# Optimization experiments

Measured on AMD Instinct MI355X. Metric: run time of the kernel, lower is better.

The kernel has to match this reference:

```python
import jax, jax.numpy as jnp
import numpy as np

B, S, D, H = 2, 2048, 1024, 16
DK = D // H


def setup_inputs() -> dict:
    key = jax.random.key(0)
    ks = jax.random.split(key, 11)
    s = 1.0 / np.sqrt(D)
    inp = {
        "q": jax.random.normal(ks[0], (B, S, D), jnp.float32),
        "k": jax.random.normal(ks[1], (B, S, D), jnp.float32),
        "v": jax.random.normal(ks[2], (B, S, D), jnp.float32),
        "mask": jnp.tril(jnp.ones((S, S), jnp.int32))[None, None],  # causal [1,1,S,S]
        "w_q": jax.random.normal(ks[3], (D, D), jnp.float32) * s,
        "b_q": jax.random.normal(ks[4], (D,), jnp.float32) * 0.01,
        "w_k": jax.random.normal(ks[5], (D, D), jnp.float32) * s,
        "b_k": jax.random.normal(ks[6], (D,), jnp.float32) * 0.01,
        "w_v": jax.random.normal(ks[7], (D, D), jnp.float32) * s,
        "b_v": jax.random.normal(ks[8], (D,), jnp.float32) * 0.01,
        "w_o": jax.random.normal(ks[9], (D, D), jnp.float32) * s,
        "b_o": jax.random.normal(ks[10], (D,), jnp.float32) * 0.01,
    }
    return inp


def reference(q, k, v, mask, w_q, b_q, w_k, b_k, w_v, b_v, w_o, b_o):
    # Linear projections (torch Linear: x @ W.T + b)
    query = q @ w_q.T + b_q  # [B,S,D]
    key_ = k @ w_k.T + b_k
    value = v @ w_v.T + b_v
    # split heads -> [B,H,S,DK]
    def split(x):
        return x.reshape(B, S, H, DK).transpose(0, 2, 1, 3)
    qh, kh, vh = split(query), split(key_), split(value)
    scores = jnp.einsum("bhqd,bhkd->bhqk", qh, kh) / jnp.sqrt(jnp.float32(DK))
    scores = jnp.where(mask == 0, jnp.float32(-1e9), scores)
    attn = jax.nn.softmax(scores, axis=-1)
    out = jnp.einsum("bhqk,bhkd->bhqd", attn, vh)  # [B,H,S,DK]
    out = out.transpose(0, 2, 1, 3).reshape(B, S, D)
    return out @ w_o.T + b_o
```

## Files before the change

kernel.cpp:

```cpp
#include <hip/hip_runtime.h>


typedef __attribute__((ext_vector_type(8))) short bf16x8;
typedef __attribute__((ext_vector_type(4))) float floatx4;
typedef __attribute__((ext_vector_type(4))) unsigned short u16x4;

#define S_LEN 2048
#define D_MODEL 1024
#define N_HEADS 16
#define D_HEAD 64
#define M_ROWS 4096
#define QSCALE 0.18033688011112042f

#define XSTR 1088
#define VSTR 4160

__device__ __forceinline__ unsigned short f32_to_bf16(float f) {
  unsigned int u = __builtin_bit_cast(unsigned int, f);
  u += 0x7FFFu + ((u >> 16) & 1u);
  return (unsigned short)(u >> 16);
}

__device__ __forceinline__ void async_lds16(const unsigned short* g, unsigned short* l) {
  __builtin_amdgcn_global_load_lds(
      (const __attribute__((address_space(1))) unsigned int*)g,
      (__attribute__((address_space(3))) unsigned int*)l, 16, 0, 0);
}

__global__ __launch_bounds__(256) void cvt_w(
    const float* __restrict__ w0, const float* __restrict__ w1,
    const float* __restrict__ w2, const float* __restrict__ w3,
    unsigned short* __restrict__ dst) {
  const int row = blockIdx.x;
  const int z = blockIdx.y;
  const float* src = ((z == 0) ? w0 : (z == 1) ? w1 : (z == 2) ? w2 : w3) + (long)row * 1024;
  unsigned short* d = dst + (long)z * 1024 * XSTR + (long)row * XSTR;
  const int tid = threadIdx.x;
  float4 f = ((const float4*)src)[tid];
  u16x4 o;
  o[0] = f32_to_bf16(f.x); o[1] = f32_to_bf16(f.y);
  o[2] = f32_to_bf16(f.z); o[3] = f32_to_bf16(f.w);
  *(u16x4*)(d + tid * 4) = o;
}

__global__ __launch_bounds__(256) void cvt_x(
    const float* __restrict__ x0, const float* __restrict__ x1,
    const float* __restrict__ x2, unsigned short* __restrict__ dst) {
  const int row = blockIdx.x;
  const int z = blockIdx.y;
  const float* src = ((z == 0) ? x0 : (z == 1) ? x1 : x2) + (long)row * 1024;
  unsigned short* d = dst + (long)z * M_ROWS * XSTR + (long)row * XSTR;
  const int tid = threadIdx.x;
  float4 f = ((const float4*)src)[tid];
  u16x4 o;
  o[0] = f32_to_bf16(f.x); o[1] = f32_to_bf16(f.y);
  o[2] = f32_to_bf16(f.z); o[3] = f32_to_bf16(f.w);
  *(u16x4*)(d + tid * 4) = o;
}

#define GK 1024
#define GN 1024

template <bool XPRE>
__global__ __launch_bounds__(256, 3) void qkv_gemm(
    const float* __restrict__ Xq, const float* __restrict__ Xk, const float* __restrict__ Xv,
    const unsigned short* __restrict__ Xb,
    const unsigned short* __restrict__ Wb,
    const float* __restrict__ bq, const float* __restrict__ bk, const float* __restrict__ bv,
    unsigned short* __restrict__ Yq, unsigned short* __restrict__ Yk,
    unsigned short* __restrict__ Yvt) {
  __shared__ __align__(16) unsigned short As[128 * 64];
  __shared__ __align__(16) unsigned short Bs[128 * 64];

  const int z = blockIdx.z;
  const unsigned short* W = Wb + (long)z * 1024 * XSTR;
  const float* bias = (z == 0) ? bq : ((z == 1) ? bk : bv);

  const int r0 = blockIdx.x * 128;
  const int n0 = blockIdx.y * 128;
  const int tid = threadIdx.x;
  const int lane = tid & 63;
  const int wave = tid >> 6;
  const int quad = lane >> 4;
  const int ln = lane & 15;
  const int wm = (wave >> 1) * 64;
  const int wn = (wave & 1) * 64;

  floatx4 acc[4][4];
#pragma unroll
  for (int i = 0; i < 4; i++)
#pragma unroll
    for (int j = 0; j < 4; j++) acc[i][j] = (floatx4){0.f, 0.f, 0.f, 0.f};

  const int srow = (lane >> 3);
  const int scol8 = (lane & 7) * 8;
  const unsigned short* ApH = nullptr;
  const float* ApF = nullptr;
  if constexpr (XPRE) {
    ApH = Xb + (long)z * M_ROWS * XSTR;
  } else {
    ApF = (z == 0) ? Xq : ((z == 1) ? Xk : Xv);
  }

  for (int k0 = 0; k0 < GK; k0 += 64) {
    __syncthreads();
    if constexpr (XPRE) {
#pragma unroll
      for (int i = 0; i < 4; i++) {
        const int row = wave * 32 + i * 8;
        async_lds16(ApH + (long)(r0 + row + srow) * XSTR + k0 + scol8,
                    As + row * 64);
        async_lds16(W + (long)(n0 + row + srow) * XSTR + k0 + scol8,
                    Bs + row * 64);
      }
    } else {
      const int arow = tid >> 1;
      const int acol = (tid & 1) * 32;
      unsigned short ua[32] __attribute__((aligned(16)));
      float fa[32] __attribute__((aligned(16)));
#pragma unroll
      for (int c = 0; c < 8; c++)
        *(float4*)(fa + c * 4) = *(const float4*)(ApF + (long)(r0 + arow) * GK + k0 + acol + c * 4);
#pragma unroll
      for (int j = 0; j < 32; j++) ua[j] = f32_to_bf16(fa[j]);
      *(float4*)(As + arow * 64 + acol) = *(float4*)(ua);
      *(float4*)(As + arow * 64 + acol + 8) = *(float4*)(ua + 8);
      *(float4*)(As + arow * 64 + acol + 16) = *(float4*)(ua + 16);
      *(float4*)(As + arow * 64 + acol + 24) = *(float4*)(ua + 24);
#pragma unroll
      for (int i = 0; i < 4; i++) {
        const int row = wave * 32 + i * 8;
        async_lds16(W + (long)(n0 + row + srow) * XSTR + k0 + scol8,
                    Bs + row * 64);
      }
    }
    __syncthreads();

#pragma unroll
    for (int ks = 0; ks < 64; ks += 32) {
      bf16x8 af[4], bfr[4];
#pragma unroll
      for (int mt = 0; mt < 4; mt++)
        af[mt] = *(const bf16x8*)(As + (wm + mt * 16 + ln) * 64 + ks + quad * 8);
#pragma unroll
      for (int nt = 0; nt < 4; nt++)
        bfr[nt] = *(const bf16x8*)(Bs + (wn + nt * 16 + ln) * 64 + ks + quad * 8);
#pragma unroll
      for (int mt = 0; mt < 4; mt++)
#pragma unroll
        for (int nt = 0; nt < 4; nt++)
          acc[mt][nt] = __builtin_amdgcn_mfma_f32_16x16x32_bf16(af[mt], bfr[nt], acc[mt][nt], 0, 0, 0);
    }
  }

#pragma unroll
  for (int nt = 0; nt < 4; nt++) {
    const int n = n0 + wn + nt * 16 + ln;
    const float bv = bias[n];
#pragma unroll
    for (int mt = 0; mt < 4; mt++) {
      const int r = r0 + wm + mt * 16 + quad * 4;
      if (z == 2) {
        u16x4 pk;
#pragma unroll
        for (int reg = 0; reg < 4; reg++) pk[reg] = f32_to_bf16(acc[mt][nt][reg] + bv);
        *(u16x4*)(Yvt + (long)n * VSTR + r) = pk;
      } else if (z == 0) {
#pragma unroll
        for (int reg = 0; reg < 4; reg++)
          Yq[(long)(r + reg) * XSTR + n] = f32_to_bf16((acc[mt][nt][reg] + bv) * QSCALE);
      } else {
#pragma unroll
        for (int reg = 0; reg < 4; reg++)
          Yk[(long)(r + reg) * XSTR + n] = f32_to_bf16(acc[mt][nt][reg] + bv);
      }
    }
  }
}

__global__ __launch_bounds__(256, 3) void out_gemm(
    const unsigned short* __restrict__ X,
    const unsigned short* __restrict__ W,
    const float* __restrict__ bias,
    float* __restrict__ Y) {
  __shared__ __align__(16) unsigned short As[64 * 64];
  __shared__ __align__(16) unsigned short Bs[128 * 64];

  const int r0 = blockIdx.x * 64;
  const int n0 = blockIdx.y * 128;
  const int tid = threadIdx.x;
  const int lane = tid & 63;
  const int wave = tid >> 6;
  const int quad = lane >> 4;
  const int ln = lane & 15;
  const int wm = (wave >> 1) * 32;
  const int wn = (wave & 1) * 64;

  floatx4 acc[2][4];
#pragma unroll
  for (int i = 0; i < 2; i++)
#pragma unroll
    for (int j = 0; j < 4; j++) acc[i][j] = (floatx4){0.f, 0.f, 0.f, 0.f};

  const int srow = (lane >> 3);
  const int scol8 = (lane & 7) * 8;

  for (int k0 = 0; k0 < GK; k0 += 64) {
    __syncthreads();
#pragma unroll
    for (int i = 0; i < 2; i++) {
      const int row = wave * 16 + i * 8;
      async_lds16(X + (long)(r0 + row + srow) * XSTR + k0 + scol8, As + row * 64);
    }
#pragma unroll
    for (int i = 0; i < 4; i++) {
      const int row = wave * 32 + i * 8;
      async_lds16(W + (long)(n0 + row + srow) * XSTR + k0 + scol8, Bs + row * 64);
    }
    __syncthreads();

#pragma unroll
    for (int ks = 0; ks < 64; ks += 32) {
      bf16x8 af[2], bfr[4];
#pragma unroll
      for (int mt = 0; mt < 2; mt++)
        af[mt] = *(const bf16x8*)(As + (wm + mt * 16 + ln) * 64 + ks + quad * 8);
#pragma unroll
      for (int nt = 0; nt < 4; nt++)
        bfr[nt] = *(const bf16x8*)(Bs + (wn + nt * 16 + ln) * 64 + ks + quad * 8);
#pragma unroll
      for (int mt = 0; mt < 2; mt++)
#pragma unroll
        for (int nt = 0; nt < 4; nt++)
          acc[mt][nt] = __builtin_amdgcn_mfma_f32_16x16x32_bf16(af[mt], bfr[nt], acc[mt][nt], 0, 0, 0);
    }
  }

#pragma unroll
  for (int nt = 0; nt < 4; nt++) {
    const int n = n0 + wn + nt * 16 + ln;
    const float bv = bias[n];
#pragma unroll
    for (int mt = 0; mt < 2; mt++) {
      const int r = r0 + wm + mt * 16 + quad * 4;
#pragma unroll
      for (int reg = 0; reg < 4; reg++)
        Y[(long)(r + reg) * GN + n] = acc[mt][nt][reg] + bv;
    }
  }
}

#define PSTR 72

__global__ __launch_bounds__(256, 3) void attn_causal(
    const unsigned short* __restrict__ Q,
    const unsigned short* __restrict__ K,
    const unsigned short* __restrict__ Vt,
    unsigned short* __restrict__ O) {
  __shared__ __align__(16) unsigned short Ks[2][64 * 64];
  __shared__ __align__(16) unsigned short Vs[2][64 * 64];
  __shared__ __align__(16) unsigned short Pb[4][16 * PSTR];

  const int g = blockIdx.x;
  const int bh = blockIdx.y;
  const int b = bh >> 4;
  const int h = bh & 15;

  const int tid = threadIdx.x;
  const int wave = tid >> 6;
  const int lane = tid & 63;
  const int quad = lane >> 4;
  const int ln = lane & 15;

  const int s = (wave < 2) ? (2 * g + wave) : (126 - 2 * g + (wave & 1));
  const int q0 = s * 16;
  const int nkt_self = (s >> 2) + 1;
  const int nkt_blk = ((127 - 2 * g) >> 2) + 1;

  const unsigned short* Qb = Q + (long)b * S_LEN * XSTR + h * D_HEAD;
  const unsigned short* Kb = K + (long)b * S_LEN * XSTR + h * D_HEAD;
  const unsigned short* Vb = Vt + (long)h * D_HEAD * VSTR + b * S_LEN;

  const int srow = tid >> 3;
  const int sslot = (tid & 7) ^ (srow & 7);
  const unsigned short* Ksrc = Kb + (long)srow * XSTR + sslot * 8;
  const unsigned short* Vsrc = Vb + (long)srow * VSTR + sslot * 8;
  unsigned short* myP = Pb[wave];
  const int swz = ln & 7;

  auto stage = [&](int buf, int kt) {
    const long kOff = (long)(kt * 64) * XSTR;
    const int vOff = kt * 64;
    async_lds16(Ksrc + kOff, &Ks[buf][wave * 512]);
    async_lds16(Ksrc + kOff + (long)32 * XSTR, &Ks[buf][2048 + wave * 512]);
    async_lds16(Vsrc + vOff, &Vs[buf][wave * 512]);
    async_lds16(Vsrc + (long)32 * VSTR + vOff, &Vs[buf][2048 + wave * 512]);
  };

  bf16x8 qf0 = *(const bf16x8*)(Qb + (long)(q0 + ln) * XSTR + quad * 8);
  bf16x8 qf1 = *(const bf16x8*)(Qb + (long)(q0 + ln) * XSTR + 32 + quad * 8);

  float m = -1e30f, l = 0.f;
  floatx4 o[4];
#pragma unroll
  for (int nt = 0; nt < 4; nt++) o[nt] = (floatx4){0.f, 0.f, 0.f, 0.f};

  auto iterate = [&](int buf, int kt) {
    const int kv0 = kt * 64;
    const unsigned short* Kt = Ks[buf];
    const unsigned short* Vtile = Vs[buf];

    floatx4 sS[4];
#pragma unroll
    for (int ct = 0; ct < 4; ct++) {
      const int row = ct * 16 + ln;
      bf16x8 k0 = *(const bf16x8*)(Kt + row * 64 + ((quad ^ swz) * 8));
      bf16x8 k1 = *(const bf16x8*)(Kt + row * 64 + (((4 + quad) ^ swz) * 8));
      sS[ct] = (floatx4){0.f, 0.f, 0.f, 0.f};
      sS[ct] = __builtin_amdgcn_mfma_f32_16x16x32_bf16(k0, qf0, sS[ct], 0, 0, 0);
      sS[ct] = __builtin_amdgcn_mfma_f32_16x16x32_bf16(k1, qf1, sS[ct], 0, 0, 0);
    }

    float tmax = -1e30f;
    if (kt == nkt_self - 1) {
      const int qg = q0 + ln;
#pragma unroll
      for (int ct = 0; ct < 4; ct++) {
        const int kvb = kv0 + ct * 16 + quad * 4;
#pragma unroll
        for (int reg = 0; reg < 4; reg++) {
          float sv = sS[ct][reg];
          if (kvb + reg > qg) sv = -1e30f;
          sS[ct][reg] = sv;
          tmax = fmaxf(tmax, sv);
        }
      }
    } else {
#pragma unroll
      for (int ct = 0; ct < 4; ct++)
#pragma unroll
        for (int reg = 0; reg < 4; reg++) tmax = fmaxf(tmax, sS[ct][reg]);
    }
    tmax = fmaxf(tmax, __shfl_xor(tmax, 16, 64));
    tmax = fmaxf(tmax, __shfl_xor(tmax, 32, 64));
    const float mnew = fmaxf(m, tmax);
    const float alpha = exp2f(m - mnew);
    m = mnew;
    float rsum = 0.f;
#pragma unroll
    for (int ct = 0; ct < 4; ct++) {
      u16x4 pk;
#pragma unroll
      for (int reg = 0; reg < 4; reg++) {
        const float p = exp2f(sS[ct][reg] - m);
        rsum += p;
        pk[reg] = f32_to_bf16(p);
      }
      *(u16x4*)(myP + ln * PSTR + ct * 16 + quad * 4) = pk;
    }
    rsum += __shfl_xor(rsum, 16, 64);
    rsum += __shfl_xor(rsum, 32, 64);
    l = l * alpha + rsum;
#pragma unroll
    for (int nt = 0; nt < 4; nt++)
#pragma unroll
      for (int reg = 0; reg < 4; reg++) o[nt][reg] *= alpha;

    __builtin_amdgcn_wave_barrier();

    bf16x8 p0 = *(const bf16x8*)(myP + ln * PSTR + quad * 8);
    bf16x8 p1 = *(const bf16x8*)(myP + ln * PSTR + 32 + quad * 8);
#pragma unroll
    for (int nt = 0; nt < 4; nt++) {
      const int row = nt * 16 + ln;
      bf16x8 v0 = *(const bf16x8*)(Vtile + row * 64 + ((quad ^ swz) * 8));
      bf16x8 v1 = *(const bf16x8*)(Vtile + row * 64 + (((4 + quad) ^ swz) * 8));
      o[nt] = __builtin_amdgcn_mfma_f32_16x16x32_bf16(v0, p0, o[nt], 0, 0, 0);
      o[nt] = __builtin_amdgcn_mfma_f32_16x16x32_bf16(v1, p1, o[nt], 0, 0, 0);
    }
    __builtin_amdgcn_wave_barrier();
  };

  stage(0, 0);
  __syncthreads();
#pragma unroll 1
  for (int kt = 0; kt < nkt_blk; kt++) {
    if (kt + 1 < nkt_blk) stage((kt + 1) & 1, kt + 1);
    if (kt < nkt_self) iterate(kt & 1, kt);
    __syncthreads();
  }

  const float inv = 1.0f / l;
  unsigned short* op = O + (long)b * S_LEN * XSTR + (long)(q0 + ln) * XSTR + h * D_HEAD;
#pragma unroll
  for (int nt = 0; nt < 4; nt++) {
    u16x4 pk;
#pragma unroll
    for (int reg = 0; reg < 4; reg++) pk[reg] = f32_to_bf16(o[nt][reg] * inv);
    *(u16x4*)(op + nt * 16 + quad * 4) = pk;
  }
}

extern "C" void kernel_launch(void* const* d_in, const int* in_sizes, int n_in,
                              void* d_out, int out_size, void* d_ws, size_t ws_size,
                              hipStream_t stream) {
  const float* q = (const float*)d_in[0];
  const float* k = (const float*)d_in[1];
  const float* v = (const float*)d_in[2];
  const float* w_q = (const float*)d_in[4];
  const float* b_q = (const float*)d_in[5];
  const float* w_k = (const float*)d_in[6];
  const float* b_k = (const float*)d_in[7];
  const float* w_v = (const float*)d_in[8];
  const float* b_v = (const float*)d_in[9];
  const float* w_o = (const float*)d_in[10];
  const float* b_o = (const float*)d_in[11];
  float* out = (float*)d_out;

  unsigned short* ws = (unsigned short*)d_ws;
  const long NR = (long)M_ROWS * XSTR;
  const long NV = (long)1024 * VSTR;
  const long NWALL = (long)4 * 1024 * XSTR;
  const long NXALL = 3 * NR;
  const long TOT_XPRE = 2 * NR + NV + NWALL + NXALL;
  const bool xpre = (ws_size >= (size_t)TOT_XPRE * sizeof(unsigned short));

  unsigned short *Qp, *Kp, *Vpt, *AO, *Wb, *Xb;
  if (xpre) {
    Qp = ws;
    Kp = ws + NR;
    Vpt = ws + 2 * NR;
    Wb = ws + 2 * NR + NV;
    Xb = Wb + NWALL;
    AO = Xb;
  } else {
    Qp = ws;
    Kp = ws + NR;
    Vpt = ws + 2 * NR;
    AO = ws + 2 * NR + NV;
    Wb = AO + NR;
    Xb = nullptr;
  }

  cvt_w<<<dim3(1024, 4), 256, 0, stream>>>(w_q, w_k, w_v, w_o, Wb);
  if (xpre) {
    cvt_x<<<dim3(4096, 3), 256, 0, stream>>>(q, k, v, Xb);
    qkv_gemm<true><<<dim3(M_ROWS / 128, GN / 128, 3), 256, 0, stream>>>(
        q, k, v, Xb, Wb, b_q, b_k, b_v, Qp, Kp, Vpt);
  } else {
    qkv_gemm<false><<<dim3(M_ROWS / 128, GN / 128, 3), 256, 0, stream>>>(
        q, k, v, nullptr, Wb, b_q, b_k, b_v, Qp, Kp, Vpt);
  }
  attn_causal<<<dim3(32, 32), 256, 0, stream>>>(Qp, Kp, Vpt, AO);
  out_gemm<<<dim3(M_ROWS / 64, GN / 128), 256, 0, stream>>>(AO, Wb + 3 * (long)1024 * XSTR, b_o, out);
}
```

Measured before the change: 274.7 us.

## Single-buffer K/V tiles in attention, raise occupancy, skip unneeded rescales

The attention kernel drops the K/V double buffer to a single LDS buffer, which halves that shared memory. It also raises the launch-bounds minimum blocks per CU from 3 to 4 to get more resident waves. The load for each tile now runs synchronously before compute behind a barrier, so copy/compute overlap is given up in the hope that extra occupancy hides the latency. It also skips the online-softmax rescale of o and l when no lane's running max changes, at the cost of a wave vote.

```diff
diff --git a/kernel.cpp b/kernel.cpp
--- a/kernel.cpp
+++ b/kernel.cpp
@@ -252,13 +252,13 @@
 
 #define PSTR 72
 
-__global__ __launch_bounds__(256, 3) void attn_causal(
+__global__ __launch_bounds__(256, 4) void attn_causal(
     const unsigned short* __restrict__ Q,
     const unsigned short* __restrict__ K,
     const unsigned short* __restrict__ Vt,
     unsigned short* __restrict__ O) {
-  __shared__ __align__(16) unsigned short Ks[2][64 * 64];
-  __shared__ __align__(16) unsigned short Vs[2][64 * 64];
+  __shared__ __align__(16) unsigned short Ks[64 * 64];
+  __shared__ __align__(16) unsigned short Vs[64 * 64];
   __shared__ __align__(16) unsigned short Pb[4][16 * PSTR];
 
   const int g = blockIdx.x;
@@ -288,13 +288,13 @@
   unsigned short* myP = Pb[wave];
   const int swz = ln & 7;
 
-  auto stage = [&](int buf, int kt) {
+  auto stage = [&](int kt) {
     const long kOff = (long)(kt * 64) * XSTR;
     const int vOff = kt * 64;
-    async_lds16(Ksrc + kOff, &Ks[buf][wave * 512]);
-    async_lds16(Ksrc + kOff + (long)32 * XSTR, &Ks[buf][2048 + wave * 512]);
-    async_lds16(Vsrc + vOff, &Vs[buf][wave * 512]);
-    async_lds16(Vsrc + (long)32 * VSTR + vOff, &Vs[buf][2048 + wave * 512]);
+    async_lds16(Ksrc + kOff, &Ks[wave * 512]);
+    async_lds16(Ksrc + kOff + (long)32 * XSTR, &Ks[2048 + wave * 512]);
+    async_lds16(Vsrc + vOff, &Vs[wave * 512]);
+    async_lds16(Vsrc + (long)32 * VSTR + vOff, &Vs[2048 + wave * 512]);
   };
 
   bf16x8 qf0 = *(const bf16x8*)(Qb + (long)(q0 + ln) * XSTR + quad * 8);
@@ -305,17 +305,15 @@
 #pragma unroll
   for (int nt = 0; nt < 4; nt++) o[nt] = (floatx4){0.f, 0.f, 0.f, 0.f};
 
-  auto iterate = [&](int buf, int kt) {
+  auto iterate = [&](int kt) {
     const int kv0 = kt * 64;
-    const unsigned short* Kt = Ks[buf];
-    const unsigned short* Vtile = Vs[buf];
 
     floatx4 sS[4];
 #pragma unroll
     for (int ct = 0; ct < 4; ct++) {
       const int row = ct * 16 + ln;
-      bf16x8 k0 = *(const bf16x8*)(Kt + row * 64 + ((quad ^ swz) * 8));
-      bf16x8 k1 = *(const bf16x8*)(Kt + row * 64 + (((4 + quad) ^ swz) * 8));
+      bf16x8 k0 = *(const bf16x8*)(Ks + row * 64 + ((quad ^ swz) * 8));
+      bf16x8 k1 = *(const bf16x8*)(Ks + row * 64 + (((4 + quad) ^ swz) * 8));
       sS[ct] = (floatx4){0.f, 0.f, 0.f, 0.f};
       sS[ct] = __builtin_amdgcn_mfma_f32_16x16x32_bf16(k0, qf0, sS[ct], 0, 0, 0);
       sS[ct] = __builtin_amdgcn_mfma_f32_16x16x32_bf16(k1, qf1, sS[ct], 0, 0, 0);
@@ -343,9 +341,16 @@
     }
     tmax = fmaxf(tmax, __shfl_xor(tmax, 16, 64));
     tmax = fmaxf(tmax, __shfl_xor(tmax, 32, 64));
-    const float mnew = fmaxf(m, tmax);
-    const float alpha = exp2f(m - mnew);
-    m = mnew;
+    if (!__all(tmax <= m)) {
+      const float mnew = fmaxf(m, tmax);
+      const float alpha = exp2f(m - mnew);
+      m = mnew;
+      l *= alpha;
+#pragma unroll
+      for (int nt = 0; nt < 4; nt++)
+#pragma unroll
+        for (int reg = 0; reg < 4; reg++) o[nt][reg] *= alpha;
+    }
     float rsum = 0.f;
 #pragma unroll
     for (int ct = 0; ct < 4; ct++) {
@@ -360,11 +365,7 @@
     }
     rsum += __shfl_xor(rsum, 16, 64);
     rsum += __shfl_xor(rsum, 32, 64);
-    l = l * alpha + rsum;
-#pragma unroll
-    for (int nt = 0; nt < 4; nt++)
-#pragma unroll
-      for (int reg = 0; reg < 4; reg++) o[nt][reg] *= alpha;
+    l += rsum;
 
     __builtin_amdgcn_wave_barrier();
 
@@ -373,20 +374,18 @@
 #pragma unroll
     for (int nt = 0; nt < 4; nt++) {
       const int row = nt * 16 + ln;
-      bf16x8 v0 = *(const bf16x8*)(Vtile + row * 64 + ((quad ^ swz) * 8));
-      bf16x8 v1 = *(const bf16x8*)(Vtile + row * 64 + (((4 + quad) ^ swz) * 8));
+      bf16x8 v0 = *(const bf16x8*)(Vs + row * 64 + ((quad ^ swz) * 8));
+      bf16x8 v1 = *(const bf16x8*)(Vs + row * 64 + (((4 + quad) ^ swz) * 8));
       o[nt] = __builtin_amdgcn_mfma_f32_16x16x32_bf16(v0, p0, o[nt], 0, 0, 0);
       o[nt] = __builtin_amdgcn_mfma_f32_16x16x32_bf16(v1, p1, o[nt], 0, 0, 0);
     }
-    __builtin_amdgcn_wave_barrier();
   };
 
-  stage(0, 0);
-  __syncthreads();
 #pragma unroll 1
   for (int kt = 0; kt < nkt_blk; kt++) {
-    if (kt + 1 < nkt_blk) stage((kt + 1) & 1, kt + 1);
-    if (kt < nkt_self) iterate(kt & 1, kt);
+    stage(kt);
+    __syncthreads();
+    if (kt < nkt_self) iterate(kt);
     __syncthreads();
   }
 
```

Result: faster. 251.0 us (-8.7%).
